# Performance work log

Hardware: AMD Instinct MI355X
Metric: run time of the kernel (lower is better)

## Reference

```python
import jax, jax.numpy as jnp
import numpy as np

N = 16      # manifold_dim
H = 128     # hidden_dim
B = 256     # batch
EPS = 1e-6


def setup_inputs() -> dict:
    key = jax.random.key(0)
    ks = jax.random.split(key, 14)
    def w(k, shape):
        fan_in = shape[0]
        return jax.random.uniform(k, shape, jnp.float32, -1.0, 1.0) / np.sqrt(fan_in)
    return {
        "points": jax.random.normal(ks[0], (B, N), jnp.float32),
        # metric network: N -> H -> N*N
        "mW1": w(ks[1], (N, H)), "mb1": jnp.zeros((H,), jnp.float32),
        "mW2": w(ks[2], (H, N * N)), "mb2": jnp.zeros((N * N,), jnp.float32),
        # christoffel network: 3 -> H -> 1
        "cW1": w(ks[3], (3, H)), "cb1": jnp.zeros((H,), jnp.float32),
        "cW2": w(ks[4], (H, 1)), "cb2": jnp.zeros((1,), jnp.float32),
        # ricci network: 4N -> 2H -> N*N
        "rW1": w(ks[5], (4 * N, 2 * H)), "rb1": jnp.zeros((2 * H,), jnp.float32),
        "rW2": w(ks[6], (2 * H, N * N)), "rb2": jnp.zeros((N * N,), jnp.float32),
    }


def reference(points, mW1, mb1, mW2, mb2, cW1, cb1, cW2, cb2, rW1, rb1, rW2, rb2):
    b = points.shape[0]
    n = N
    # ---- metric: (b, n, n) ----
    mh = jax.nn.relu(points @ mW1 + mb1)
    metric = (mh @ mW2 + mb2).reshape(b, n, n)
    metric = metric + EPS * jnp.eye(n, dtype=metric.dtype)
    metric = 0.5 * (metric + jnp.swapaxes(metric, -2, -1))

    # ---- christoffel: vectorized over all (i,j,k) triples ----
    # inputs per triple: [metric_ij, metric_jk, metric_ki]
    m_ij = jnp.broadcast_to(metric[:, :, :, None], (b, n, n, n))
    m_jk = jnp.broadcast_to(metric[:, None, :, :], (b, n, n, n))
    mT = jnp.swapaxes(metric, -2, -1)  # mT[b,i,k] = metric[b,k,i]
    m_ki = jnp.broadcast_to(mT[:, :, None, :], (b, n, n, n))
    ch_in = jnp.stack([m_ij, m_jk, m_ki], axis=-1)        # (b,n,n,n,3)
    ch_h = jnp.tanh(ch_in @ cW1 + cb1)                    # (b,n,n,n,H)
    christoffel = (ch_h @ cW2 + cb2)[..., 0]              # (b,n,n,n)

    # ---- ricci: vectorized over all (i,j) pairs ----
    p_b = jnp.broadcast_to(points[:, None, None, :], (b, n, n, n))
    m_i = jnp.broadcast_to(metric[:, :, None, :], (b, n, n, n))
    m_j = jnp.broadcast_to(metric[:, None, :, :], (b, n, n, n))
    r_in = jnp.concatenate([p_b, m_i, m_j, christoffel], axis=-1)  # (b,n,n,4n)
    r_h = jax.nn.relu(r_in @ rW1 + rb1)                   # (b,n,n,2H)
    r_out = (r_h @ rW2 + rb2).reshape(b, n, n, n, n)      # (b,i,j,n,n)
    r_out = 0.5 * (r_out + jnp.swapaxes(r_out, -1, -2))
    ricci = r_out.sum(axis=(1, 2)) / (n * n)              # (b,n,n)
    return ricci
```

## Files before the change

kernel.cpp:

```cpp
#include <hip/hip_runtime.h>
#include <hip/hip_bf16.h>

#define NDIM 16
#define HDIM 128
#define BATCH 256
#define EPS_D 1e-6f

typedef float v2f __attribute__((ext_vector_type(2)));
static __device__ __forceinline__ v2f v2(float a, float b) {
  v2f r; r.x = a; r.y = b; return r;
}
static __device__ __forceinline__ v2f splat(float a) {
  v2f r; r.x = a; r.y = a; return r;
}

__global__ __launch_bounds__(256) void metric_proj_kernel(
    const float* __restrict__ points,
    const float* __restrict__ mW1, const float* __restrict__ mb1,
    const float* __restrict__ mW2, const float* __restrict__ mb2,
    const float* __restrict__ rW1, const float* __restrict__ rb1,
    float* __restrict__ metric,
    float* __restrict__ A1, float* __restrict__ Mi, float* __restrict__ Mj,
    float* __restrict__ G) {
  int b = blockIdx.x;
  int t = threadIdx.x;
  __shared__ float p[16];
  __shared__ float mh[128];
  __shared__ float raw[256];
  __shared__ float M[256];
  G[b * 256 + t] = 0.f;
  if (t < 16) p[t] = points[b * 16 + t];
  __syncthreads();
  if (t < 128) {
    float acc = mb1[t];
#pragma unroll
    for (int k = 0; k < 16; ++k) acc = fmaf(p[k], mW1[k * 128 + t], acc);
    mh[t] = fmaxf(acc, 0.f);
  }
  __syncthreads();
  {
    float acc = mb2[t];
#pragma unroll 8
    for (int h = 0; h < 128; ++h) acc = fmaf(mh[h], mW2[h * 256 + t], acc);
    raw[t] = acc;
  }
  __syncthreads();
  {
    int i = t >> 4, j = t & 15;
    float v = 0.5f * (raw[i * 16 + j] + raw[j * 16 + i]);
    if (i == j) v += EPS_D;
    M[t] = v;
    metric[b * 256 + t] = v;
  }
  __syncthreads();
  {
    int h = t;
    float wB[16], wC[16];
#pragma unroll
    for (int c = 0; c < 16; ++c) {
      wB[c] = rW1[(16 + c) * 256 + h];
      wC[c] = rW1[(32 + c) * 256 + h];
    }
    float a = rb1[h];
#pragma unroll
    for (int r = 0; r < 16; ++r) a = fmaf(p[r], rW1[r * 256 + h], a);
    A1[b * 256 + h] = a;
#pragma unroll 2
    for (int i = 0; i < 16; ++i) {
      float mi = 0.f, mj = 0.f;
#pragma unroll
      for (int c = 0; c < 16; ++c) {
        float m = M[i * 16 + c];
        mi = fmaf(m, wB[c], mi);
        mj = fmaf(m, wC[c], mj);
      }
      Mi[(b * 16 + i) * 256 + h] = mi;
      Mj[(b * 16 + i) * 256 + h] = mj;
    }
  }
}

__global__ __launch_bounds__(128, 6) void chr_kernel(
    const float* __restrict__ metric,
    const float* __restrict__ cW1, const float* __restrict__ cb1,
    const float* __restrict__ cW2, const float* __restrict__ cb2,
    const float* __restrict__ rW1,
    const float* __restrict__ A1, const float* __restrict__ Mi,
    const float* __restrict__ Mj,
    float* __restrict__ G) {
  int bi = blockIdx.x;
  int b = bi >> 4, i = bi & 15;
  int t = threadIdx.x;
  int w = t >> 6, l = t & 63;
  __shared__ float M[256];
  __shared__ float4 z[128];
  __shared__ float4 w2p[32];
  __shared__ float4 ch4[64];
  float* chf = (float*)ch4;
  M[t] = metric[b * 256 + t];
  M[t + 128] = metric[b * 256 + t + 128];
  {
    const float S = 2.8853900817779268f;
    z[t] = make_float4(S * cW1[t], S * cW1[128 + t], S * cW1[256 + t],
                       S * cb1[t]);
    ((float*)w2p)[t] = cW2[t];
  }
  __syncthreads();

  {
    int jk0 = w * 128 + l, jk1 = jk0 + 64;
    int j0 = jk0 >> 4, k0 = jk0 & 15;
    int j1 = jk1 >> 4, k1 = jk1 & 15;
    v2f x0 = v2(M[i * 16 + j0], M[i * 16 + j1]);
    v2f x1 = v2(M[j0 * 16 + k0], M[j1 * 16 + k1]);
    v2f x2 = v2(M[k0 * 16 + i], M[k1 * 16 + i]);
    v2f acc = splat(cb2[0]);
    for (int hq = 0; hq < 32; ++hq) {
      float4 W2 = w2p[hq];
      float w2u[4] = {W2.x, W2.y, W2.z, W2.w};
#pragma unroll
      for (int u = 0; u < 4; ++u) {
        float4 Q = z[hq * 4 + u];
        v2f pre = __builtin_elementwise_fma(
            x0, splat(Q.x),
            __builtin_elementwise_fma(
                x1, splat(Q.y),
                __builtin_elementwise_fma(x2, splat(Q.z), splat(Q.w))));
        v2f e;
        e.x = __builtin_amdgcn_exp2f(pre.x);
        e.y = __builtin_amdgcn_exp2f(pre.y);
        v2f ep = e + splat(1.f);
        v2f r;
        r.x = __builtin_amdgcn_rcpf(ep.x);
        r.y = __builtin_amdgcn_rcpf(ep.y);
        v2f th = __builtin_elementwise_fma(splat(-2.f), r, splat(1.f));
        acc = __builtin_elementwise_fma(th, splat(w2u[u]), acc);
      }
    }
    chf[jk0] = acc.x;
    chf[jk1] = acc.y;
  }
  __syncthreads();

  {
    int h0 = w * 128 + l, h1 = h0 + 64;
    v2f rc2[16];
#pragma unroll
    for (int kk = 0; kk < 16; ++kk)
      rc2[kk] = v2(rW1[(48 + kk) * 256 + h0], rW1[(48 + kk) * 256 + h1]);
    v2f base = v2(A1[b * 256 + h0] + Mi[bi * 256 + h0],
                  A1[b * 256 + h1] + Mi[bi * 256 + h1]);
    v2f hacc = splat(0.f);
    for (int jj = 0; jj < 16; ++jj) {
      float4 c0 = ch4[jj * 4 + 0];
      float4 c1 = ch4[jj * 4 + 1];
      float4 c2v = ch4[jj * 4 + 2];
      float4 c3 = ch4[jj * 4 + 3];
      v2f mj = v2(Mj[(b * 16 + jj) * 256 + h0], Mj[(b * 16 + jj) * 256 + h1]);
      v2f cp = base + mj;
      float cc[16] = {c0.x, c0.y, c0.z, c0.w, c1.x, c1.y, c1.z, c1.w,
                      c2v.x, c2v.y, c2v.z, c2v.w, c3.x, c3.y, c3.z, c3.w};
#pragma unroll
      for (int kk = 0; kk < 16; ++kk)
        cp = __builtin_elementwise_fma(splat(cc[kk]), rc2[kk], cp);
      v2f rl;
      rl.x = fmaxf(cp.x, 0.f);
      rl.y = fmaxf(cp.y, 0.f);
      hacc += rl;
    }
    atomicAdd(&G[b * 256 + h0], hacc.x);
    atomicAdd(&G[b * 256 + h1], hacc.y);
  }
}

__global__ __launch_bounds__(256) void final_kernel(
    const float* __restrict__ G,
    const float* __restrict__ rW2, const float* __restrict__ rb2,
    float* __restrict__ out) {
  int b = blockIdx.x;
  int t = threadIdx.x;
  __shared__ float4 Gs[64];
  __shared__ float T[256];
  if (t < 64) Gs[t] = ((const float4*)(G + b * 256))[t];
  __syncthreads();
  float acc = 256.f * rb2[t];
#pragma unroll 4
  for (int h4 = 0; h4 < 64; ++h4) {
    float4 gg = Gs[h4];
    acc = fmaf(gg.x, rW2[(h4 * 4 + 0) * 256 + t], acc);
    acc = fmaf(gg.y, rW2[(h4 * 4 + 1) * 256 + t], acc);
    acc = fmaf(gg.z, rW2[(h4 * 4 + 2) * 256 + t], acc);
    acc = fmaf(gg.w, rW2[(h4 * 4 + 3) * 256 + t], acc);
  }
  T[t] = acc * (1.f / 256.f);
  __syncthreads();
  int k = t >> 4, lcol = t & 15;
  out[b * 256 + t] = 0.5f * (T[k * 16 + lcol] + T[lcol * 16 + k]);
}

extern "C" void kernel_launch(void* const* d_in, const int* in_sizes, int n_in,
                              void* d_out, int out_size, void* d_ws, size_t ws_size,
                              hipStream_t stream) {
  const float* points = (const float*)d_in[0];
  const float* mW1 = (const float*)d_in[1];
  const float* mb1 = (const float*)d_in[2];
  const float* mW2 = (const float*)d_in[3];
  const float* mb2 = (const float*)d_in[4];
  const float* cW1 = (const float*)d_in[5];
  const float* cb1 = (const float*)d_in[6];
  const float* cW2 = (const float*)d_in[7];
  const float* cb2 = (const float*)d_in[8];
  const float* rW1 = (const float*)d_in[9];
  const float* rb1 = (const float*)d_in[10];
  const float* rW2 = (const float*)d_in[11];
  const float* rb2 = (const float*)d_in[12];
  float* out = (float*)d_out;

  float* ws = (float*)d_ws;
  float* metric = ws;
  float* A1 = metric + 65536;
  float* Mi = A1 + 65536;
  float* Mj = Mi + 1048576;
  float* G = Mj + 1048576;

  metric_proj_kernel<<<BATCH, 256, 0, stream>>>(points, mW1, mb1, mW2, mb2,
                                                rW1, rb1, metric, A1, Mi, Mj, G);
  chr_kernel<<<BATCH * NDIM, 128, 0, stream>>>(metric, cW1, cb1, cW2, cb2, rW1,
                                               A1, Mi, Mj, G);
  final_kernel<<<BATCH, 256, 0, stream>>>(G, rW2, rb2, out);
}
```

Before: 133.7 us.

## Fuse final projection into chr kernel via last-block counter; share reciprocal across tanh pairs

The final rW2 projection kernel is removed. In chr_kernel, the last of the 16 blocks for each batch row (found with an acq_rel atomic counter) reads the accumulated G and computes the symmetrized output. This saves one kernel launch and its dependency gap. The tanh loop now computes four reciprocals from one rcp of a product of the denominators, cutting transcendental instructions in exchange for a few extra multiplies and a higher risk of overflow or precision loss. The tail work runs on only 256 blocks of 128 threads while other blocks may already be finished.

Result: slower. 219.3 us (+64.0%).

```diff
diff --git a/kernel.cpp b/kernel.cpp
--- a/kernel.cpp
+++ b/kernel.cpp
@@ -21,7 +21,7 @@
     const float* __restrict__ rW1, const float* __restrict__ rb1,
     float* __restrict__ metric,
     float* __restrict__ A1, float* __restrict__ Mi, float* __restrict__ Mj,
-    float* __restrict__ G) {
+    float* __restrict__ G, int* __restrict__ cnt) {
   int b = blockIdx.x;
   int t = threadIdx.x;
   __shared__ float p[16];
@@ -29,6 +29,7 @@
   __shared__ float raw[256];
   __shared__ float M[256];
   G[b * 256 + t] = 0.f;
+  if (t == 0) cnt[b] = 0;
   if (t < 16) p[t] = points[b * 16 + t];
   __syncthreads();
   if (t < 128) {
@@ -87,7 +88,9 @@
     const float* __restrict__ rW1,
     const float* __restrict__ A1, const float* __restrict__ Mi,
     const float* __restrict__ Mj,
-    float* __restrict__ G) {
+    const float* __restrict__ rW2, const float* __restrict__ rb2,
+    float* __restrict__ G, int* __restrict__ cnt,
+    float* __restrict__ out) {
   int bi = blockIdx.x;
   int b = bi >> 4, i = bi & 15;
   int t = threadIdx.x;
@@ -96,6 +99,7 @@
   __shared__ float4 z[128];
   __shared__ float4 w2p[32];
   __shared__ float4 ch4[64];
+  __shared__ int lastFlag;
   float* chf = (float*)ch4;
   M[t] = metric[b * 256 + t];
   M[t + 128] = metric[b * 256 + t + 128];
@@ -119,22 +123,37 @@
       float4 W2 = w2p[hq];
       float w2u[4] = {W2.x, W2.y, W2.z, W2.w};
 #pragma unroll
-      for (int u = 0; u < 4; ++u) {
-        float4 Q = z[hq * 4 + u];
-        v2f pre = __builtin_elementwise_fma(
-            x0, splat(Q.x),
+      for (int up = 0; up < 2; ++up) {
+        float4 Q0 = z[hq * 4 + 2 * up];
+        float4 Q1 = z[hq * 4 + 2 * up + 1];
+        v2f pre0 = __builtin_elementwise_fma(
+            x0, splat(Q0.x),
             __builtin_elementwise_fma(
-                x1, splat(Q.y),
-                __builtin_elementwise_fma(x2, splat(Q.z), splat(Q.w))));
-        v2f e;
-        e.x = __builtin_amdgcn_exp2f(pre.x);
-        e.y = __builtin_amdgcn_exp2f(pre.y);
-        v2f ep = e + splat(1.f);
-        v2f r;
-        r.x = __builtin_amdgcn_rcpf(ep.x);
-        r.y = __builtin_amdgcn_rcpf(ep.y);
-        v2f th = __builtin_elementwise_fma(splat(-2.f), r, splat(1.f));
-        acc = __builtin_elementwise_fma(th, splat(w2u[u]), acc);
+                x1, splat(Q0.y),
+                __builtin_elementwise_fma(x2, splat(Q0.z), splat(Q0.w))));
+        v2f pre1 = __builtin_elementwise_fma(
+            x0, splat(Q1.x),
+            __builtin_elementwise_fma(
+                x1, splat(Q1.y),
+                __builtin_elementwise_fma(x2, splat(Q1.z), splat(Q1.w))));
+        v2f eA, eB;
+        eA.x = __builtin_amdgcn_exp2f(pre0.x);
+        eA.y = __builtin_amdgcn_exp2f(pre0.y);
+        eB.x = __builtin_amdgcn_exp2f(pre1.x);
+        eB.y = __builtin_amdgcn_exp2f(pre1.y);
+        v2f epA = eA + splat(1.f);
+        v2f epB = eB + splat(1.f);
+        v2f P = epA * epB;
+        float s = P.x * P.y;
+        float R = __builtin_amdgcn_rcpf(s);
+        v2f Psw; Psw.x = P.y; Psw.y = P.x;
+        v2f invP = Psw * splat(R);
+        v2f rA = epB * invP;
+        v2f rB = epA * invP;
+        v2f thA = __builtin_elementwise_fma(splat(-2.f), rA, splat(1.f));
+        v2f thB = __builtin_elementwise_fma(splat(-2.f), rB, splat(1.f));
+        acc = __builtin_elementwise_fma(thA, splat(w2u[2 * up]), acc);
+        acc = __builtin_elementwise_fma(thB, splat(w2u[2 * up + 1]), acc);
       }
     }
     chf[jk0] = acc.x;
@@ -142,8 +161,8 @@
   }
   __syncthreads();
 
-  {
-    int h0 = w * 128 + l, h1 = h0 + 64;
+  int h0 = w * 128 + l, h1 = h0 + 64;
+  {
     v2f rc2[16];
 #pragma unroll
     for (int kk = 0; kk < 16; ++kk)
@@ -171,31 +190,43 @@
     atomicAdd(&G[b * 256 + h0], hacc.x);
     atomicAdd(&G[b * 256 + h1], hacc.y);
   }
-}
-
-__global__ __launch_bounds__(256) void final_kernel(
-    const float* __restrict__ G,
-    const float* __restrict__ rW2, const float* __restrict__ rb2,
-    float* __restrict__ out) {
-  int b = blockIdx.x;
-  int t = threadIdx.x;
-  __shared__ float4 Gs[64];
-  __shared__ float T[256];
-  if (t < 64) Gs[t] = ((const float4*)(G + b * 256))[t];
-  __syncthreads();
-  float acc = 256.f * rb2[t];
+
+  __syncthreads();
+  if (t == 0) {
+    int old = __hip_atomic_fetch_add(&cnt[b], 1, __ATOMIC_ACQ_REL,
+                                     __HIP_MEMORY_SCOPE_AGENT);
+    lastFlag = (old == 15);
+  }
+  __syncthreads();
+  if (lastFlag) {
+    float* Gl = M;
+    Gl[t] = __hip_atomic_load(&G[b * 256 + t], __ATOMIC_RELAXED,
+                              __HIP_MEMORY_SCOPE_AGENT);
+    Gl[t + 128] = __hip_atomic_load(&G[b * 256 + 128 + t], __ATOMIC_RELAXED,
+                                    __HIP_MEMORY_SCOPE_AGENT);
+    __syncthreads();
+    int t2 = t + 128;
+    float acc0 = 256.f * rb2[t];
+    float acc1 = 256.f * rb2[t2];
 #pragma unroll 4
-  for (int h4 = 0; h4 < 64; ++h4) {
-    float4 gg = Gs[h4];
-    acc = fmaf(gg.x, rW2[(h4 * 4 + 0) * 256 + t], acc);
-    acc = fmaf(gg.y, rW2[(h4 * 4 + 1) * 256 + t], acc);
-    acc = fmaf(gg.z, rW2[(h4 * 4 + 2) * 256 + t], acc);
-    acc = fmaf(gg.w, rW2[(h4 * 4 + 3) * 256 + t], acc);
-  }
-  T[t] = acc * (1.f / 256.f);
-  __syncthreads();
-  int k = t >> 4, lcol = t & 15;
-  out[b * 256 + t] = 0.5f * (T[k * 16 + lcol] + T[lcol * 16 + k]);
+    for (int h = 0; h < 256; ++h) {
+      float gh = Gl[h];
+      acc0 = fmaf(gh, rW2[h * 256 + t], acc0);
+      acc1 = fmaf(gh, rW2[h * 256 + t2], acc1);
+    }
+    float* Tl = chf;
+    Tl[t] = acc0 * (1.f / 256.f);
+    Tl[t2] = acc1 * (1.f / 256.f);
+    __syncthreads();
+    {
+      int k = t >> 4, lcol = t & 15;
+      out[b * 256 + t] = 0.5f * (Tl[k * 16 + lcol] + Tl[lcol * 16 + k]);
+    }
+    {
+      int k = t2 >> 4, lcol = t2 & 15;
+      out[b * 256 + t2] = 0.5f * (Tl[k * 16 + lcol] + Tl[lcol * 16 + k]);
+    }
+  }
 }
 
 extern "C" void kernel_launch(void* const* d_in, const int* in_sizes, int n_in,
@@ -222,10 +253,12 @@
   float* Mi = A1 + 65536;
   float* Mj = Mi + 1048576;
   float* G = Mj + 1048576;
+  int* cnt = (int*)(G + 65536);
 
   metric_proj_kernel<<<BATCH, 256, 0, stream>>>(points, mW1, mb1, mW2, mb2,
-                                                rW1, rb1, metric, A1, Mi, Mj, G);
+                                                rW1, rb1, metric, A1, Mi, Mj,
+                                                G, cnt);
   chr_kernel<<<BATCH * NDIM, 128, 0, stream>>>(metric, cW1, cb1, cW2, cb2, rW1,
-                                               A1, Mi, Mj, G);
-  final_kernel<<<BATCH, 256, 0, stream>>>(G, rW2, rb2, out);
-}
+                                               A1, Mi, Mj, rW2, rb2, G, cnt,
+                                               out);
+}
```
